# Performance work log

Measured on AMD Instinct MI355X. Metric: run time of the kernel, lower is better.

The kernel has to match this reference:

```python
import jax, jax.numpy as jnp
import numpy as np


def setup_inputs() -> dict:
    key = jax.random.key(0)
    k1, k2 = jax.random.split(key)
    B, C, H, W = 8, 64, 128, 256
    src = jax.random.normal(k1, (B, C, H, W), dtype=jnp.float32)
    tgt = jax.random.normal(k2, (B, C, H, W), dtype=jnp.float32)
    return {"src": src, "tgt": tgt, "search_range": 4}


def reference(src, tgt, search_range):
    # Cost volume: for each (dy, dx) shift of tgt (zero-padded), channel dot with src.
    # Output channel ordering matches the torch loop: center, then for i=1..S:
    # (+i,0), (-i,0), (0,+i), (0,-i), then for j=1..S: (+i,+j), (-i,+j), (+i,-j), (-i,-j).
    S = search_range
    B, C, H, W = src.shape
    tgt_pad = jnp.pad(tgt, ((0, 0), (0, 0), (S, S), (S, S)))

    def cost(di, dj):
        # shifted[y, x] = tgt[y - di, x - dj] (zero outside)
        shifted = tgt_pad[:, :, S - di:S - di + H, S - dj:S - dj + W]
        return jnp.sum(shifted * src, axis=1)  # [B, H, W]

    outs = [cost(0, 0)]
    for i in range(1, S + 1):
        outs.extend([cost(i, 0), cost(-i, 0), cost(0, i), cost(0, -i)])
        for j in range(1, S + 1):
            outs.extend([cost(i, j), cost(-i, j), cost(i, -j), cost(-i, -j)])
    return jnp.stack(outs, axis=1)  # [B, (2S+1)^2, H, W]
```

## Files before the change

### kernel.cpp

```cpp
#include <hip/hip_runtime.h>

#define S    4
#define BB   8
#define CC   64
#define HH   128
#define WW   256
#define KCH  16
#define NCP  8
#define TH   4
#define TW   64
#define PX   4
#define NTX  16
#define TROWS 12
#define PITCHD 72
#define NT   576
#define NCH  (CC / KCH)
#define HW   (HH * WW)
#define TGTU (NCP * TROWS * 18)
#define SRCU (NCP * TH * 16)

typedef _Float16 h2 __attribute__((ext_vector_type(2)));

#if __has_builtin(__builtin_amdgcn_cvt_pkrtz)
__device__ inline h2 pack2(float x, float y) {
  return __builtin_bit_cast(h2, __builtin_amdgcn_cvt_pkrtz(x, y));
}
#else
__device__ inline h2 pack2(float x, float y) { h2 r; r[0] = (_Float16)x; r[1] = (_Float16)y; return r; }
#endif

#if __has_builtin(__builtin_amdgcn_fdot2)
__device__ inline float dot2(h2 a, h2 b, float c) { return __builtin_amdgcn_fdot2(a, b, c, false); }
#else
__device__ inline float dot2(h2 a, h2 b, float c) { return c + (float)a[0]*(float)b[0] + (float)a[1]*(float)b[1]; }
#endif

__device__ __host__ constexpr int ord_idx(int di, int dj) {
  int i = di < 0 ? -di : di;
  int j = dj < 0 ? -dj : dj;
  if (i == 0 && j == 0) return 0;
  if (j == 0) return 1 + (i - 1) * 20 + (di > 0 ? 0 : 1);
  if (i == 0) return 1 + (j - 1) * 20 + (dj > 0 ? 2 : 3);
  return 1 + (i - 1) * 20 + 4 + (j - 1) * 4 +
         (di > 0 ? (dj > 0 ? 0 : 2) : (dj > 0 ? 1 : 3));
}

__global__ __launch_bounds__(NT, 4)
void costvol_kernel(const float* __restrict__ src,
                    const float* __restrict__ tgt,
                    float* __restrict__ out) {
  __shared__ __align__(16) float lds2[NCP * TROWS * PITCHD];
  __shared__ __align__(16) float ldss[NCP * TH * 64];

  const int tx  = threadIdx.x;
  const int ty  = threadIdx.y;
  const int tz  = threadIdx.z;
  const int tid = tz * 64 + ty * 16 + tx;
  const int bx  = blockIdx.x;
  const int by  = blockIdx.y;
  const int b   = blockIdx.z;

  const int w0b = bx * TW;
  const int h0  = by * TH;
  const int h   = h0 + ty;
  const int w0  = w0b + tx * PX;
  const int di  = tz - S;
  const int row = ty - tz + 8;

  int lofs[3], goff[3];
#pragma unroll
  for (int k = 0; k < 3; ++k) {
    const int u   = tid + k * NT;
    const int cp  = u / (TROWS * 18);
    const int rem = u - cp * (TROWS * 18);
    const int r   = rem / 18;
    const int wq  = rem - r * 18;
    const int gh  = h0 - S + r;
    const int gw  = w0b - S + 4 * wq;
    lofs[k] = cp * (TROWS * PITCHD) + r * PITCHD + 4 * wq;
    goff[k] = -1;
    if ((unsigned)gh < (unsigned)HH && gw >= 0 && gw + 3 < WW)
      goff[k] = ((b * CC + 2 * cp) * HW) + gh * WW + gw;
  }

  const int scp = tid >> 6;
  const int sr  = (tid >> 4) & 3;
  const int sq  = tid & 15;
  const int sgo = (b * CC + 2 * scp) * HW + (h0 + sr) * WW + w0b + 4 * sq;
  const int slo = (scp * TH + sr) * 64 + 4 * sq;

  float acc[9][PX];
#pragma unroll
  for (int o = 0; o < 9; ++o)
#pragma unroll
    for (int p = 0; p < PX; ++p) acc[o][p] = 0.f;

  float4 tA[3], tB[3], sA, sB;
  const float4 z4 = make_float4(0.f, 0.f, 0.f, 0.f);

#define ISSUE(CHN) do {                                                     \
    const int _off = (CHN) * (KCH * HW);                                    \
    _Pragma("unroll")                                                       \
    for (int k = 0; k < 3; ++k) {                                           \
      tA[k] = z4; tB[k] = z4;                                               \
      if (goff[k] >= 0) {                                                   \
        tA[k] = *reinterpret_cast<const float4*>(tgt + goff[k] + _off);     \
        tB[k] = *reinterpret_cast<const float4*>(tgt + goff[k] + _off + HW);\
      }                                                                     \
    }                                                                       \
    if (tid < SRCU) {                                                       \
      sA = *reinterpret_cast<const float4*>(src + sgo + _off);              \
      sB = *reinterpret_cast<const float4*>(src + sgo + _off + HW);         \
    }                                                                       \
  } while (0)

  ISSUE(0);

  for (int ch = 0; ch < NCH; ++ch) {
#pragma unroll
    for (int k = 0; k < 3; ++k) {
      float4 wv;
      wv.x = __builtin_bit_cast(float, pack2(tA[k].x, tB[k].x));
      wv.y = __builtin_bit_cast(float, pack2(tA[k].y, tB[k].y));
      wv.z = __builtin_bit_cast(float, pack2(tA[k].z, tB[k].z));
      wv.w = __builtin_bit_cast(float, pack2(tA[k].w, tB[k].w));
      *reinterpret_cast<float4*>(lds2 + lofs[k]) = wv;
    }
    if (tid < SRCU) {
      float4 wv;
      wv.x = __builtin_bit_cast(float, pack2(sA.x, sB.x));
      wv.y = __builtin_bit_cast(float, pack2(sA.y, sB.y));
      wv.z = __builtin_bit_cast(float, pack2(sA.z, sB.z));
      wv.w = __builtin_bit_cast(float, pack2(sA.w, sB.w));
      *reinterpret_cast<float4*>(ldss + slo) = wv;
    }

    __syncthreads();

    if (ch + 1 < NCH) ISSUE(ch + 1);

#pragma unroll
    for (int cp = 0; cp < NCP; ++cp) {
      const float4 st = *reinterpret_cast<const float4*>(
          ldss + (cp * TH + ty) * 64 + 4 * tx);
      const h2 sv[PX] = {__builtin_bit_cast(h2, st.x), __builtin_bit_cast(h2, st.y),
                         __builtin_bit_cast(h2, st.z), __builtin_bit_cast(h2, st.w)};

      const float* lp = lds2 + cp * (TROWS * PITCHD) + row * PITCHD + 4 * tx;
      h2 win[12];
#pragma unroll
      for (int q = 0; q < 3; ++q) {
        const float4 t = *reinterpret_cast<const float4*>(lp + 4 * q);
        win[4 * q]     = __builtin_bit_cast(h2, t.x);
        win[4 * q + 1] = __builtin_bit_cast(h2, t.y);
        win[4 * q + 2] = __builtin_bit_cast(h2, t.z);
        win[4 * q + 3] = __builtin_bit_cast(h2, t.w);
      }

#pragma unroll
      for (int dj = -S; dj <= S; ++dj) {
#pragma unroll
        for (int p = 0; p < PX; ++p)
          acc[dj + S][p] = dot2(sv[p], win[p - dj + 4], acc[dj + S][p]);
      }
    }

    __syncthreads();
  }

  const size_t HWs = (size_t)HW;
  float* op = out + (size_t)b * 81 * HWs + (size_t)h * WW + w0;
#pragma unroll
  for (int dj = -S; dj <= S; ++dj) {
    const int o    = ord_idx(di, dj);
    const int slot = dj + S;
    *reinterpret_cast<float4*>(op + (size_t)o * HWs) =
        make_float4(acc[slot][0], acc[slot][1], acc[slot][2], acc[slot][3]);
  }
}

extern "C" void kernel_launch(void* const* d_in, const int* in_sizes, int n_in,
                              void* d_out, int out_size, void* d_ws, size_t ws_size,
                              hipStream_t stream) {
  const float* src = (const float*)d_in[0];
  const float* tgt = (const float*)d_in[1];
  float* out = (float*)d_out;
  dim3 grid(WW / TW, HH / TH, BB);
  dim3 block(NTX, TH, 9);
  costvol_kernel<<<grid, block, 0, stream>>>(src, tgt, out);
}
```

Baseline: 71.56 us.

## Double-buffer LDS with halved channel chunks and one barrier per iteration

Cuts the per-iteration channel chunk from 16 to 8 channels and double-buffers the shared-memory tiles, so only one __syncthreads is needed per iteration instead of two. The next chunk's global loads are issued before the barrier. This is meant to remove barrier stalls and overlap loads with compute. The cost is twice as many loop iterations, each doing less work, plus changed load bookkeeping and fewer per-thread load registers.

Measured after the change: 67.58 us. 5.6% less time.

```diff
diff --git a/kernel.cpp b/kernel.cpp
--- a/kernel.cpp
+++ b/kernel.cpp
@@ -5,8 +5,8 @@
 #define CC   64
 #define HH   128
 #define WW   256
-#define KCH  16
-#define NCP  8
+#define KCH  8
+#define NCP  4
 #define TH   4
 #define TW   64
 #define PX   4
@@ -18,6 +18,8 @@
 #define HW   (HH * WW)
 #define TGTU (NCP * TROWS * 18)
 #define SRCU (NCP * TH * 16)
+#define L2SZ (NCP * TROWS * PITCHD)
+#define LSSZ (NCP * TH * 64)
 
 typedef _Float16 h2 __attribute__((ext_vector_type(2)));
 
@@ -49,8 +51,8 @@
 void costvol_kernel(const float* __restrict__ src,
                     const float* __restrict__ tgt,
                     float* __restrict__ out) {
-  __shared__ __align__(16) float lds2[NCP * TROWS * PITCHD];
-  __shared__ __align__(16) float ldss[NCP * TH * 64];
+  __shared__ __align__(16) float lds2[2][L2SZ];
+  __shared__ __align__(16) float ldss[2][LSSZ];
 
   const int tx  = threadIdx.x;
   const int ty  = threadIdx.y;
@@ -67,23 +69,26 @@
   const int di  = tz - S;
   const int row = ty - tz + 8;
 
-  int lofs[3], goff[3];
+  int lofs0 = -1, goff0 = -1, lofs1 = -1, goff1 = -1;
 #pragma unroll
-  for (int k = 0; k < 3; ++k) {
-    const int u   = tid + k * NT;
-    const int cp  = u / (TROWS * 18);
-    const int rem = u - cp * (TROWS * 18);
-    const int r   = rem / 18;
-    const int wq  = rem - r * 18;
-    const int gh  = h0 - S + r;
-    const int gw  = w0b - S + 4 * wq;
-    lofs[k] = cp * (TROWS * PITCHD) + r * PITCHD + 4 * wq;
-    goff[k] = -1;
-    if ((unsigned)gh < (unsigned)HH && gw >= 0 && gw + 3 < WW)
-      goff[k] = ((b * CC + 2 * cp) * HW) + gh * WW + gw;
+  for (int k = 0; k < 2; ++k) {
+    const int u = tid + k * NT;
+    if (u < TGTU) {
+      const int cp  = u / (TROWS * 18);
+      const int rem = u - cp * (TROWS * 18);
+      const int r   = rem / 18;
+      const int wq  = rem - r * 18;
+      const int gh  = h0 - S + r;
+      const int gw  = w0b - S + 4 * wq;
+      const int lo  = cp * (TROWS * PITCHD) + r * PITCHD + 4 * wq;
+      int go = -1;
+      if ((unsigned)gh < (unsigned)HH && gw >= 0 && gw + 3 < WW)
+        go = ((b * CC + 2 * cp) * HW) + gh * WW + gw;
+      if (k == 0) { lofs0 = lo; goff0 = go; } else { lofs1 = lo; goff1 = go; }
+    }
   }
 
-  const int scp = tid >> 6;
+  const int scp = (tid >> 6) & 3;
   const int sr  = (tid >> 4) & 3;
   const int sq  = tid & 15;
   const int sgo = (b * CC + 2 * scp) * HW + (h0 + sr) * WW + w0b + 4 * sq;
@@ -95,18 +100,19 @@
 #pragma unroll
     for (int p = 0; p < PX; ++p) acc[o][p] = 0.f;
 
-  float4 tA[3], tB[3], sA, sB;
+  float4 tA0, tB0, tA1, tB1, sA, sB;
   const float4 z4 = make_float4(0.f, 0.f, 0.f, 0.f);
 
 #define ISSUE(CHN) do {                                                     \
     const int _off = (CHN) * (KCH * HW);                                    \
-    _Pragma("unroll")                                                       \
-    for (int k = 0; k < 3; ++k) {                                           \
-      tA[k] = z4; tB[k] = z4;                                               \
-      if (goff[k] >= 0) {                                                   \
-        tA[k] = *reinterpret_cast<const float4*>(tgt + goff[k] + _off);     \
-        tB[k] = *reinterpret_cast<const float4*>(tgt + goff[k] + _off + HW);\
-      }                                                                     \
+    tA0 = z4; tB0 = z4; tA1 = z4; tB1 = z4;                                 \
+    if (goff0 >= 0) {                                                       \
+      tA0 = *reinterpret_cast<const float4*>(tgt + goff0 + _off);           \
+      tB0 = *reinterpret_cast<const float4*>(tgt + goff0 + _off + HW);      \
+    }                                                                       \
+    if (goff1 >= 0) {                                                       \
+      tA1 = *reinterpret_cast<const float4*>(tgt + goff1 + _off);           \
+      tB1 = *reinterpret_cast<const float4*>(tgt + goff1 + _off + HW);      \
     }                                                                       \
     if (tid < SRCU) {                                                       \
       sA = *reinterpret_cast<const float4*>(src + sgo + _off);              \
@@ -114,39 +120,39 @@
     }                                                                       \
   } while (0)
 
+#define PACKQ(VA, VB, DST) do {                                             \
+    float4 _wv;                                                             \
+    _wv.x = __builtin_bit_cast(float, pack2((VA).x, (VB).x));               \
+    _wv.y = __builtin_bit_cast(float, pack2((VA).y, (VB).y));               \
+    _wv.z = __builtin_bit_cast(float, pack2((VA).z, (VB).z));               \
+    _wv.w = __builtin_bit_cast(float, pack2((VA).w, (VB).w));               \
+    *reinterpret_cast<float4*>(DST) = _wv;                                  \
+  } while (0)
+
   ISSUE(0);
 
+  int s = 0;
   for (int ch = 0; ch < NCH; ++ch) {
-#pragma unroll
-    for (int k = 0; k < 3; ++k) {
-      float4 wv;
-      wv.x = __builtin_bit_cast(float, pack2(tA[k].x, tB[k].x));
-      wv.y = __builtin_bit_cast(float, pack2(tA[k].y, tB[k].y));
-      wv.z = __builtin_bit_cast(float, pack2(tA[k].z, tB[k].z));
-      wv.w = __builtin_bit_cast(float, pack2(tA[k].w, tB[k].w));
-      *reinterpret_cast<float4*>(lds2 + lofs[k]) = wv;
-    }
-    if (tid < SRCU) {
-      float4 wv;
-      wv.x = __builtin_bit_cast(float, pack2(sA.x, sB.x));
-      wv.y = __builtin_bit_cast(float, pack2(sA.y, sB.y));
-      wv.z = __builtin_bit_cast(float, pack2(sA.z, sB.z));
-      wv.w = __builtin_bit_cast(float, pack2(sA.w, sB.w));
-      *reinterpret_cast<float4*>(ldss + slo) = wv;
-    }
+    float* lb2w = &lds2[0][0] + s * L2SZ;
+    float* lbsw = &ldss[0][0] + s * LSSZ;
+    if (lofs0 >= 0) PACKQ(tA0, tB0, lb2w + lofs0);
+    if (lofs1 >= 0) PACKQ(tA1, tB1, lb2w + lofs1);
+    if (tid < SRCU) PACKQ(sA, sB, lbsw + slo);
+
+    if (ch + 1 < NCH) ISSUE(ch + 1);
 
     __syncthreads();
 
-    if (ch + 1 < NCH) ISSUE(ch + 1);
-
+    const float* lb2 = &lds2[0][0] + s * L2SZ;
+    const float* lbs = &ldss[0][0] + s * LSSZ;
 #pragma unroll
     for (int cp = 0; cp < NCP; ++cp) {
       const float4 st = *reinterpret_cast<const float4*>(
-          ldss + (cp * TH + ty) * 64 + 4 * tx);
+          lbs + (cp * TH + ty) * 64 + 4 * tx);
       const h2 sv[PX] = {__builtin_bit_cast(h2, st.x), __builtin_bit_cast(h2, st.y),
                          __builtin_bit_cast(h2, st.z), __builtin_bit_cast(h2, st.w)};
 
-      const float* lp = lds2 + cp * (TROWS * PITCHD) + row * PITCHD + 4 * tx;
+      const float* lp = lb2 + cp * (TROWS * PITCHD) + row * PITCHD + 4 * tx;
       h2 win[12];
 #pragma unroll
       for (int q = 0; q < 3; ++q) {
@@ -165,7 +171,7 @@
       }
     }
 
-    __syncthreads();
+    s ^= 1;
   }
 
   const size_t HWs = (size_t)HW;
```
